# Optimization experiments

Measured on AMD Instinct MI355X. Metric: run time of the kernel, lower is better.

The kernel has to match this reference:

```python
import jax, jax.numpy as jnp
import numpy as np

BANDS, ROWS, SIM_THRESH = 16, 8, 0.5


def setup_inputs() -> dict:
    key = jax.random.key(0)
    k1, k2 = jax.random.split(key)
    N, D = 8192, 256
    Z = jax.random.normal(k1, (N, D), dtype=jnp.float32)
    # random hyperplanes ~ N(0, I), (bands*rows, D) -- sampled once (torch samples in forward)
    planes = jax.random.normal(k2, (BANDS * ROWS, D), dtype=jnp.float32)
    return {"Z": Z, "planes": planes}


def reference(Z, planes):
    N, D = Z.shape
    # signature: sign of projections, (bands, rows, N); +/-1 vs bool is equivalent for bucketing
    sig_bits = (planes @ Z.T >= 0).reshape(BANDS, ROWS, N)
    # bit-pack each band's row-signature into an integer key == hashing the signature bytes
    bit_weights = (2 ** jnp.arange(ROWS)).astype(jnp.int32)
    keys = jnp.einsum('brn,r->bn', sig_bits.astype(jnp.int32), bit_weights)  # (bands, N)
    # cosine pairwise similarity (row-normalized GEMM)
    Zn = Z / jnp.linalg.norm(Z, axis=1, keepdims=True)
    sim = Zn @ Zn.T  # (N, N)
    # number of bands in which i and j fall in the same LSH bucket
    def band_match(acc, k):
        return acc + (k[:, None] == k[None, :]).astype(jnp.float32), None
    counts, _ = jax.lax.scan(band_match, jnp.zeros((N, N), jnp.float32), keys)
    # original masks the diagonal with -inf, thresholds at sim_thresh, and emits one
    # (sim) entry per matching band into an uncoalesced sparse tensor; densified this
    # is counts * sim on surviving off-diagonal pairs.
    mask = (sim >= SIM_THRESH) & (~jnp.eye(N, dtype=bool))
    return jnp.where(mask, counts * sim, 0.0)
```

## Files before the change

kernel.cpp:

```cpp
#include <hip/hip_runtime.h>

typedef __attribute__((ext_vector_type(4))) float floatx4;

#define N_PTS 8192
#define D_DIM 256
#define N_PLANES 128
#define NTILE 64

__device__ inline int zbytes(unsigned int w) {
    unsigned int t = ((w & 0x7f7f7f7fu) + 0x7f7f7f7fu) | w | 0x7f7f7f7fu;
    return __popc(~t);
}

__device__ inline void load_lds16(const void* g, void* l) {
    __builtin_amdgcn_global_load_lds(
        (const __attribute__((address_space(1))) unsigned int*)g,
        (__attribute__((address_space(3))) unsigned int*)l, 16, 0, 0);
}

__global__ __launch_bounds__(256) void keys_norm_kernel(
    const float* __restrict__ Z, const float* __restrict__ planes,
    unsigned int* __restrict__ keys4, unsigned char* __restrict__ Zn) {
    __shared__ __align__(16) float zs[16][D_DIM];
    int t = threadIdx.x;
    int base = blockIdx.x * 16;

    const float4* zsrc = (const float4*)(Z + (size_t)base * D_DIM);
    float4* zdst = (float4*)&zs[0][0];
#pragma unroll
    for (int i = 0; i < 4; ++i) zdst[t + i * 256] = zsrc[t + i * 256];
    __syncthreads();

    {
        int row = t >> 4, ch = t & 15;
        const float* zr = &zs[row][ch * 16];
        float ss = 0.f;
#pragma unroll
        for (int i = 0; i < 16; ++i) ss += zr[i] * zr[i];
#pragma unroll
        for (int off = 8; off > 0; off >>= 1) ss += __shfl_xor(ss, off);
        float inv = rsqrtf(ss);
        int4 o;
#pragma unroll
        for (int q = 0; q < 4; ++q) {
            int p = __builtin_amdgcn_cvt_pk_fp8_f32(zr[q * 4] * inv,
                                                    zr[q * 4 + 1] * inv, 0, false);
            p = __builtin_amdgcn_cvt_pk_fp8_f32(zr[q * 4 + 2] * inv,
                                                zr[q * 4 + 3] * inv, p, true);
            ((int*)&o)[q] = p;
        }
        *(int4*)(Zn + (size_t)(base + row) * D_DIM + ch * 16) = o;
    }

    int p = t & 127;
    int hf = t >> 7;
    int wave = t >> 6, lane = t & 63;
    const float4* pr = (const float4*)(planes + (size_t)p * D_DIM);

    float acc[8] = {};
    for (int kk = 0; kk < D_DIM / 4; ++kk) {
        float4 pv = pr[kk];
#pragma unroll
        for (int j = 0; j < 8; ++j) {
            float4 zv = *(const float4*)&zs[hf * 8 + j][kk * 4];
            acc[j] += pv.x * zv.x + pv.y * zv.y + pv.z * zv.z + pv.w * zv.w;
        }
    }

#pragma unroll
    for (int j = 0; j < 8; ++j) {
        unsigned long long mask = __ballot(acc[j] >= 0.0f);
        if (lane < 2) {
            keys4[(size_t)(base + hf * 8 + j) * 4 + (wave & 1) * 2 + lane] =
                (unsigned int)(mask >> (32 * lane));
        }
    }
}

__global__ __launch_bounds__(256, 4) void gemm_kernel(
    const unsigned char* __restrict__ Zn, const uint4* __restrict__ keys,
    float* __restrict__ out) {
    __shared__ __align__(16) unsigned char As[16384];
    __shared__ __align__(16) unsigned char Bs[16384];
    __shared__ uint4 krow[128];
    __shared__ uint4 kcol[128];

    int idx = blockIdx.x;
    int bi = (int)((129.0f - sqrtf(16641.0f - 8.0f * (float)idx)) * 0.5f);
    while ((bi + 1) * NTILE - ((bi + 1) * bi) / 2 <= idx) ++bi;
    while (bi * NTILE - (bi * (bi - 1)) / 2 > idx) --bi;
    int bj = bi + (idx - (bi * NTILE - (bi * (bi - 1)) / 2));
    int rowBase = bi * 128;
    int colBase = bj * 128;
    bool diag = (bi == bj);

    int t = threadIdx.x;
    if (t < 128)
        krow[t] = keys[rowBase + t];
    else
        kcol[t - 128] = keys[colBase + (t - 128)];

    const unsigned char* ZnA = Zn + (size_t)rowBase * D_DIM;
    const unsigned char* ZnB = Zn + (size_t)colBase * D_DIM;

    int wave = t >> 6, lane = t & 63;
    int wm = wave >> 1, wn = wave & 1;
    int quad = lane >> 4, l16 = lane & 15;

    float* ownQ = out + (size_t)(rowBase + wm * 64 + quad * 16) * N_PTS +
                  colBase + wn * 64 + l16 * 4;
    float* mirQ = out + (size_t)(colBase + wn * 64 + quad * 16) * N_PTS +
                  rowBase + wm * 64 + l16 * 4;
    floatx4 z4 = {0.f, 0.f, 0.f, 0.f};

    floatx4 acc[4][4] = {};

    for (int s = 0; s < 2; ++s) {
        __syncthreads();
#pragma unroll
        for (int i = 0; i < 4; ++i) {
            int sa = i * 256 + t;
            int c = sa >> 7, row = sa & 127;
            size_t gOff = (size_t)row * D_DIM + s * 128 + c * 16;
            load_lds16(ZnA + gOff, &As[sa * 16]);
            load_lds16(ZnB + gOff, &Bs[sa * 16]);
        }
        if (s == 0) {
#pragma unroll
            for (int i = 0; i < 16; ++i)
                __builtin_nontemporal_store(z4, (floatx4*)(ownQ + (size_t)i * N_PTS));
        } else if (!diag) {
#pragma unroll
            for (int i = 0; i < 16; ++i)
                __builtin_nontemporal_store(z4, (floatx4*)(mirQ + (size_t)i * N_PTS));
        }
        __syncthreads();

#pragma unroll
        for (int k2 = 0; k2 < 4; ++k2) {
            int kByte = k2 * 32 + quad * 8;
            int cc = kByte >> 4;
            int off8 = kByte & 8;
            long afr[4], bfr[4];
#pragma unroll
            for (int mt = 0; mt < 4; ++mt)
                afr[mt] = *(const long*)&As[(cc * 128 + wm * 64 + mt * 16 + l16) * 16 + off8];
#pragma unroll
            for (int nt = 0; nt < 4; ++nt)
                bfr[nt] = *(const long*)&Bs[(cc * 128 + wn * 64 + nt * 16 + l16) * 16 + off8];
#pragma unroll
            for (int mt = 0; mt < 4; ++mt)
#pragma unroll
                for (int nt = 0; nt < 4; ++nt)
                    acc[mt][nt] = __builtin_amdgcn_mfma_f32_16x16x32_fp8_fp8(
                        afr[mt], bfr[nt], acc[mt][nt], 0, 0, 0);
        }
    }

    int dscal = colBase - rowBase;
    float m = 0.f;
#pragma unroll
    for (int mt = 0; mt < 4; ++mt)
#pragma unroll
        for (int nt = 0; nt < 4; ++nt)
#pragma unroll
            for (int r = 0; r < 4; ++r) {
                int liL = wm * 64 + mt * 16 + quad * 4 + r;
                int lj = wn * 64 + nt * 16 + l16;
                float x = ((lj - liL) != dscal) ? acc[mt][nt][r] : 0.f;
                m = fmaxf(m, x);
            }

    if (__ballot(m >= 0.5f)) {
#pragma unroll
        for (int mt = 0; mt < 4; ++mt)
#pragma unroll
            for (int nt = 0; nt < 4; ++nt) {
                int lj = wn * 64 + nt * 16 + l16;
                int gj = colBase + lj;
                uint4 kj = kcol[lj];
#pragma unroll
                for (int r = 0; r < 4; ++r) {
                    int liL = wm * 64 + mt * 16 + quad * 4 + r;
                    int gi = rowBase + liL;
                    float s = acc[mt][nt][r];
                    if (s >= 0.5f && gi != gj) {
                        uint4 ki = krow[liL];
                        int c = zbytes(ki.x ^ kj.x) + zbytes(ki.y ^ kj.y) +
                                zbytes(ki.z ^ kj.z) + zbytes(ki.w ^ kj.w);
                        float v = s * (float)c;
                        out[(size_t)gi * N_PTS + gj] = v;
                        if (!diag) out[(size_t)gj * N_PTS + gi] = v;
                    }
                }
            }
    }
}

extern "C" void kernel_launch(void* const* d_in, const int* in_sizes, int n_in,
                              void* d_out, int out_size, void* d_ws,
                              size_t ws_size, hipStream_t stream) {
    const float* Z = (const float*)d_in[0];
    const float* planes = (const float*)d_in[1];
    float* out = (float*)d_out;

    unsigned char* Zn = (unsigned char*)d_ws;
    unsigned int* keys4 =
        (unsigned int*)((char*)d_ws + (size_t)N_PTS * D_DIM);

    keys_norm_kernel<<<N_PTS / 16, 256, 0, stream>>>(Z, planes, keys4, Zn);
    int nblocks = NTILE * (NTILE + 1) / 2;
    gemm_kernel<<<nblocks, 256, 0, stream>>>(Zn, (const uint4*)keys4, out);
}
```

Baseline: 300.2 us.

## Zero output with linear slab stores and defer nonzero writes to scatter pass

Output zeroing moves from per-tile strided row stores into linear 128KB slabs written by the first 2048 blocks of the GEMM kernel. Surviving entries are no longer written in place. They go to a global record list through an atomic counter, and a third kernel scatters them after zeroing is done. The aim is more coalesced zero writes and no race between zeroing and value writes, at the cost of atomic contention, an extra launch, and silently dropped entries if the record buffer overflows.

```diff
diff --git a/kernel.cpp b/kernel.cpp
--- a/kernel.cpp
+++ b/kernel.cpp
@@ -20,10 +20,12 @@
 
 __global__ __launch_bounds__(256) void keys_norm_kernel(
     const float* __restrict__ Z, const float* __restrict__ planes,
-    unsigned int* __restrict__ keys4, unsigned char* __restrict__ Zn) {
+    unsigned int* __restrict__ keys4, unsigned char* __restrict__ Zn,
+    unsigned int* __restrict__ cnt) {
     __shared__ __align__(16) float zs[16][D_DIM];
     int t = threadIdx.x;
     int base = blockIdx.x * 16;
+    if (blockIdx.x == 0 && t == 0) *cnt = 0;
 
     const float4* zsrc = (const float4*)(Z + (size_t)base * D_DIM);
     float4* zdst = (float4*)&zs[0][0];
@@ -79,13 +81,24 @@
 
 __global__ __launch_bounds__(256, 4) void gemm_kernel(
     const unsigned char* __restrict__ Zn, const uint4* __restrict__ keys,
-    float* __restrict__ out) {
+    float* __restrict__ out, unsigned int* __restrict__ cnt,
+    int* __restrict__ recs, unsigned int recCap) {
     __shared__ __align__(16) unsigned char As[16384];
     __shared__ __align__(16) unsigned char Bs[16384];
     __shared__ uint4 krow[128];
     __shared__ uint4 kcol[128];
 
     int idx = blockIdx.x;
+    int t = threadIdx.x;
+
+    if (idx < 2048) {
+        float* slab = out + (size_t)idx * 32768 + t * 4;
+        floatx4 z4 = {0.f, 0.f, 0.f, 0.f};
+#pragma unroll
+        for (int i = 0; i < 32; ++i)
+            __builtin_nontemporal_store(z4, (floatx4*)(slab + i * 1024));
+    }
+
     int bi = (int)((129.0f - sqrtf(16641.0f - 8.0f * (float)idx)) * 0.5f);
     while ((bi + 1) * NTILE - ((bi + 1) * bi) / 2 <= idx) ++bi;
     while (bi * NTILE - (bi * (bi - 1)) / 2 > idx) --bi;
@@ -94,7 +107,6 @@
     int colBase = bj * 128;
     bool diag = (bi == bj);
 
-    int t = threadIdx.x;
     if (t < 128)
         krow[t] = keys[rowBase + t];
     else
@@ -106,12 +118,6 @@
     int wave = t >> 6, lane = t & 63;
     int wm = wave >> 1, wn = wave & 1;
     int quad = lane >> 4, l16 = lane & 15;
-
-    float* ownQ = out + (size_t)(rowBase + wm * 64 + quad * 16) * N_PTS +
-                  colBase + wn * 64 + l16 * 4;
-    float* mirQ = out + (size_t)(colBase + wn * 64 + quad * 16) * N_PTS +
-                  rowBase + wm * 64 + l16 * 4;
-    floatx4 z4 = {0.f, 0.f, 0.f, 0.f};
 
     floatx4 acc[4][4] = {};
 
@@ -124,15 +130,6 @@
             size_t gOff = (size_t)row * D_DIM + s * 128 + c * 16;
             load_lds16(ZnA + gOff, &As[sa * 16]);
             load_lds16(ZnB + gOff, &Bs[sa * 16]);
-        }
-        if (s == 0) {
-#pragma unroll
-            for (int i = 0; i < 16; ++i)
-                __builtin_nontemporal_store(z4, (floatx4*)(ownQ + (size_t)i * N_PTS));
-        } else if (!diag) {
-#pragma unroll
-            for (int i = 0; i < 16; ++i)
-                __builtin_nontemporal_store(z4, (floatx4*)(mirQ + (size_t)i * N_PTS));
         }
         __syncthreads();
 
@@ -189,11 +186,34 @@
                         int c = zbytes(ki.x ^ kj.x) + zbytes(ki.y ^ kj.y) +
                                 zbytes(ki.z ^ kj.z) + zbytes(ki.w ^ kj.w);
                         float v = s * (float)c;
-                        out[(size_t)gi * N_PTS + gj] = v;
-                        if (!diag) out[(size_t)gj * N_PTS + gi] = v;
+                        unsigned int n = atomicAdd(cnt, diag ? 1u : 2u);
+                        if (n < recCap) {
+                            recs[n * 3] = gi;
+                            recs[n * 3 + 1] = gj;
+                            ((float*)recs)[n * 3 + 2] = v;
+                        }
+                        if (!diag && n + 1 < recCap) {
+                            recs[(n + 1) * 3] = gj;
+                            recs[(n + 1) * 3 + 1] = gi;
+                            ((float*)recs)[(n + 1) * 3 + 2] = v;
+                        }
                     }
                 }
             }
+    }
+}
+
+__global__ __launch_bounds__(256) void scatter_kernel(
+    const int* __restrict__ recs, const unsigned int* __restrict__ cnt,
+    unsigned int recCap, float* __restrict__ out) {
+    unsigned int n = *cnt;
+    if (n > recCap) n = recCap;
+    for (unsigned int i = blockIdx.x * 256 + threadIdx.x; i < n;
+         i += gridDim.x * 256) {
+        int gi = recs[i * 3];
+        int gj = recs[i * 3 + 1];
+        float v = ((const float*)recs)[i * 3 + 2];
+        out[(size_t)gi * N_PTS + gj] = v;
     }
 }
 
@@ -207,8 +227,13 @@
     unsigned char* Zn = (unsigned char*)d_ws;
     unsigned int* keys4 =
         (unsigned int*)((char*)d_ws + (size_t)N_PTS * D_DIM);
-
-    keys_norm_kernel<<<N_PTS / 16, 256, 0, stream>>>(Z, planes, keys4, Zn);
+    unsigned int* cnt = (unsigned int*)((char*)d_ws + 2228224);
+    int* recs = (int*)((char*)d_ws + 2228480);
+    unsigned int recCap = (unsigned int)((ws_size - 2228480) / 12);
+
+    keys_norm_kernel<<<N_PTS / 16, 256, 0, stream>>>(Z, planes, keys4, Zn, cnt);
     int nblocks = NTILE * (NTILE + 1) / 2;
-    gemm_kernel<<<nblocks, 256, 0, stream>>>(Zn, (const uint4*)keys4, out);
-}
+    gemm_kernel<<<nblocks, 256, 0, stream>>>(Zn, (const uint4*)keys4, out, cnt,
+                                             recs, recCap);
+    scatter_kernel<<<256, 256, 0, stream>>>(recs, cnt, recCap, out);
+}
```

Result: slower. 313.5 us (+4.4%).
